# Kernel optimization log

Measured on AMD Instinct MI355X. Metric: run time of the kernel, lower is better.

Reference implementation:

```python
import jax, jax.numpy as jnp
import numpy as np

B, N, D, OUT = 32, 4096, 512, 512
LN_EPS = 1e-5
EPS = 1e-8


def _layernorm(x, g, b):
    m = jnp.mean(x, axis=-1, keepdims=True)
    v = jnp.mean((x - m) ** 2, axis=-1, keepdims=True)
    return (x - m) * jax.lax.rsqrt(v + LN_EPS) * g + b


def setup_inputs() -> dict:
    key = jax.random.key(0)
    ks = jax.random.split(key, 12)
    x = jax.random.normal(ks[0], (B, N, D), dtype=jnp.float32)
    mask = jax.random.bernoulli(ks[1], 0.9, (B, N))
    mask = mask.at[:, 0].set(True)  # guarantee no fully-masked row
    h = D // 4
    s = lambda fan_in: 1.0 / np.sqrt(fan_in)
    return {
        "x": x,
        "mask": mask,
        # attention MLP: Linear(D, D//4) -> tanh -> Linear(D//4, 1)
        "attn_w1": jax.random.normal(ks[2], (D, h), jnp.float32) * s(D),
        "attn_b1": jnp.zeros((h,), jnp.float32),
        "attn_w2": jax.random.normal(ks[3], (h, 1), jnp.float32) * s(h),
        "attn_b2": jnp.zeros((1,), jnp.float32),
        # gate: Linear(3D, D) -> LN -> GELU -> Linear(D, 3) -> softmax
        "gate_w1": jax.random.normal(ks[4], (3 * D, D), jnp.float32) * s(3 * D),
        "gate_b1": jnp.zeros((D,), jnp.float32),
        "gate_ln_g": jnp.ones((D,), jnp.float32),
        "gate_ln_b": jnp.zeros((D,), jnp.float32),
        "gate_w2": jax.random.normal(ks[5], (D, 3), jnp.float32) * s(D),
        "gate_b2": jnp.zeros((3,), jnp.float32),
        # out_proj: Linear(D, OUT) -> LN -> Dropout(eval: identity)
        "out_w": jax.random.normal(ks[6], (D, OUT), jnp.float32) * s(D),
        "out_b": jnp.zeros((OUT,), jnp.float32),
        "out_ln_g": jnp.ones((OUT,), jnp.float32),
        "out_ln_b": jnp.zeros((OUT,), jnp.float32),
    }


def reference(x, mask, attn_w1, attn_b1, attn_w2, attn_b2,
              gate_w1, gate_b1, gate_ln_g, gate_ln_b, gate_w2, gate_b2,
              out_w, out_b, out_ln_g, out_ln_b):
    # attention scores: [B, N]
    h = jnp.tanh(jnp.einsum('bnd,dh->bnh', x, attn_w1) + attn_b1)
    scores = (jnp.einsum('bnh,ho->bno', h, attn_w2) + attn_b2)[..., 0]
    scores = jnp.where(mask, scores, -jnp.inf)
    attn_w = jax.nn.softmax(scores, axis=-1)
    attn_w = jnp.nan_to_num(attn_w, nan=0.0)
    attn_pooled = jnp.einsum('bnd,bn->bd', x, attn_w)

    # masked max pool
    x_masked = jnp.where(mask[..., None], x, -jnp.inf)
    max_pooled = jnp.max(x_masked, axis=1)
    max_pooled = jnp.nan_to_num(max_pooled, nan=0.0, posinf=0.0, neginf=0.0)

    # masked mean pool
    mfl = mask.astype(x.dtype)
    masked_sum = jnp.einsum('bnd,bn->bd', x, mfl)
    num_valid = jnp.clip(jnp.sum(mfl, axis=1, keepdims=True), EPS, None)
    mean_pooled = masked_sum / num_valid

    # gated combine
    combined = jnp.concatenate([attn_pooled, max_pooled, mean_pooled], axis=-1)
    g = combined @ gate_w1 + gate_b1
    g = _layernorm(g, gate_ln_g, gate_ln_b)
    g = jax.nn.gelu(g, approximate=False)
    gates = jax.nn.softmax(g @ gate_w2 + gate_b2, axis=-1)  # [B, 3]

    stacked = jnp.stack([attn_pooled, max_pooled, mean_pooled], axis=2)  # [B, D, 3]
    weighted = jnp.einsum('bdk,bk->bd', stacked, gates)

    out = weighted @ out_w + out_b
    out = _layernorm(out, out_ln_g, out_ln_b)  # dropout: eval mode -> identity
    return out
```

## Files before the change

### kernel.cpp

```cpp
#include <hip/hip_runtime.h>
#include <hip/hip_bf16.h>
#include <math.h>

#define BB 32
#define NN 4096
#define DD 512
#define HH 128
#define NCH 128
#define LN_EPS 1e-5f
#define MEPS 1e-8f

typedef __attribute__((ext_vector_type(8))) short bf16x8;
typedef __attribute__((ext_vector_type(4))) float f32x4;

__device__ __forceinline__ unsigned pk_bf16(float a, float b) {
    unsigned ua = __float_as_uint(a); ua = (ua + 0x7FFFu + ((ua >> 16) & 1u)) >> 16;
    unsigned ub = __float_as_uint(b); ub = (ub + 0x7FFFu + ((ub >> 16) & 1u)) >> 16;
    return ua | (ub << 16);
}
__device__ __forceinline__ unsigned short bf16_1(float a) {
    unsigned ua = __float_as_uint(a);
    return (unsigned short)((ua + 0x7FFFu + ((ua >> 16) & 1u)) >> 16);
}
__device__ __forceinline__ float bflo(unsigned u) { return __uint_as_float(u << 16); }
__device__ __forceinline__ float bfhi(unsigned u) { return __uint_as_float(u & 0xFFFF0000u); }

__global__ __launch_bounds__(256) void gmsp_prep(
    const void* __restrict__ mask, unsigned char* __restrict__ m8,
    const float* __restrict__ w1, unsigned short* __restrict__ w1f)
{
    int blk = blockIdx.x, t = threadIdx.x;
    if (blk < 512) {
        __shared__ int sf[2];
        const unsigned* mu = (const unsigned*)mask;
        bool f32f = false, i8f = false;
#pragma unroll
        for (int i = 0; i < 4; ++i) {
            unsigned v = mu[t + i * 256];
            f32f |= (v == 0x3F800000u);
            i8f  |= (v > 1u) && (v != 0x3F800000u);
        }
        if (t == 0) { sf[0] = 0; sf[1] = 0; }
        __syncthreads();
        int wf32 = __any((int)f32f), wi8 = __any((int)i8f);
        if ((t & 63) == 0) {
            if (wf32) atomicOr(&sf[0], 1);
            if (wi8)  atomicOr(&sf[1], 1);
        }
        __syncthreads();
        int fmt = sf[0] ? 2 : (sf[1] ? 1 : 0);
        int i = blk * 256 + t;
        unsigned char v;
        if (fmt == 1)      v = ((const unsigned char*)mask)[i] != 0;
        else if (fmt == 2) v = ((const float*)mask)[i] != 0.0f;
        else               v = ((const int*)mask)[i] != 0;
        m8[i] = v;
    } else {
        int idx = (blk - 512) * 256 + t;
        int j = idx & 7;
        int e = idx >> 3;
        int lane = e & 63;
        int half = (e >> 6) & 1;
        int s = (e >> 7) & 15;
        int g2 = (e >> 11) & 3;
        int h = g2 * 32 + half * 16 + (lane & 15);
        int k = s * 32 + (lane >> 4) * 8 + j;
        w1f[(size_t)e * 8 + j] = bf16_1(w1[(size_t)k * HH + h]);
    }
}

__global__ __launch_bounds__(256, 1) void gmsp_fused(
    const float* __restrict__ x, const unsigned short* __restrict__ w1f,
    const float* __restrict__ b1, const float* __restrict__ w2,
    const float* __restrict__ b2, const unsigned char* __restrict__ m8,
    float* __restrict__ attnp, float* __restrict__ sump, float* __restrict__ maxp,
    float* __restrict__ mc, float* __restrict__ sc, float* __restrict__ cnt)
{
    __shared__ char At[32 * 1024];
    __shared__ float sred[32][4] __attribute__((aligned(16)));
    __shared__ float wrow[32];
    __shared__ float cpool[2][512];

    const int t = threadIdx.x;
    const int lane = t & 63, wid = t >> 6;
    const int l15 = lane & 15, lq = (lane >> 4) & 3;
    const int blk = blockIdx.x;
    const int b = blk >> 7, ch = blk & 127;
    const size_t row0 = (size_t)b * NN + (size_t)ch * 32;

    float4 sreg[16];
    {
        const float4* xb = (const float4*)(x + row0 * DD);
#pragma unroll
        for (int j = 0; j < 16; ++j) sreg[j] = xb[j * 256 + t];
    }
    uint4 mq0 = *(const uint4*)(m8 + row0);
    uint4 mq1 = *(const uint4*)(m8 + row0 + 16);
    unsigned mwa[8] = {mq0.x, mq0.y, mq0.z, mq0.w, mq1.x, mq1.y, mq1.z, mq1.w};

    const int H = t >> 7;
    const int c4 = t & 127;
    float ps[4] = {0.f, 0.f, 0.f, 0.f};
    float pm[4] = {-INFINITY, -INFINITY, -INFINITY, -INFINITY};
#pragma unroll
    for (int j = 0; j < 16; ++j) {
        const int row = 2 * j + H;
        float4 v = sreg[j];
        uint2 pw; pw.x = pk_bf16(v.x, v.y); pw.y = pk_bf16(v.z, v.w);
        *(uint2*)(At + row * 1024 + ((c4 * 8) ^ ((row & 7) << 4))) = pw;
        int mv = (mwa[j >> 1] >> ((2 * (j & 1) + H) * 8)) & 0xFF;
        if (mv) {
            ps[0] += v.x; ps[1] += v.y; ps[2] += v.z; ps[3] += v.w;
            pm[0] = fmaxf(pm[0], v.x); pm[1] = fmaxf(pm[1], v.y);
            pm[2] = fmaxf(pm[2], v.z); pm[3] = fmaxf(pm[3], v.w);
        }
    }
    __syncthreads();

    const int hb = wid * 32;
    f32x4 acc00 = (f32x4)0.f, acc01 = (f32x4)0.f, acc10 = (f32x4)0.f, acc11 = (f32x4)0.f;
    {
        const char* wf = (const char*)w1f + (size_t)wid * 32768 + (size_t)lane * 16;
        const char* ar0 = At + l15 * 1024;
        const char* ar1 = At + (16 + l15) * 1024;
        const int swz = (l15 & 7) << 4;
#pragma unroll
        for (int s = 0; s < 16; ++s) {
            bf16x8 bf0 = *(const bf16x8*)(wf + s * 2048);
            bf16x8 bf1 = *(const bf16x8*)(wf + s * 2048 + 1024);
            const int co = (s * 64 + lq * 16) ^ swz;
            bf16x8 a0 = *(const bf16x8*)(ar0 + co);
            bf16x8 a1 = *(const bf16x8*)(ar1 + co);
            acc00 = __builtin_amdgcn_mfma_f32_16x16x32_bf16(a0, bf0, acc00, 0, 0, 0);
            acc01 = __builtin_amdgcn_mfma_f32_16x16x32_bf16(a0, bf1, acc01, 0, 0, 0);
            acc10 = __builtin_amdgcn_mfma_f32_16x16x32_bf16(a1, bf0, acc10, 0, 0, 0);
            acc11 = __builtin_amdgcn_mfma_f32_16x16x32_bf16(a1, bf1, acc11, 0, 0, 0);
        }
    }
    {
        const float b10 = b1[hb + l15], b11 = b1[hb + 16 + l15];
        const float w20 = w2[hb + l15], w21 = w2[hb + 16 + l15];
#pragma unroll
        for (int rf = 0; rf < 2; ++rf) {
            f32x4 aA = rf ? acc10 : acc00;
            f32x4 aB = rf ? acc11 : acc01;
#pragma unroll
            for (int r = 0; r < 4; ++r) {
                float p0 = fminf(fmaxf(aA[r] + b10, -10.f), 10.f);
                float p1 = fminf(fmaxf(aB[r] + b11, -10.f), 10.f);
                float e0 = __expf(2.f * p0), e1 = __expf(2.f * p1);
                float v = (e0 - 1.f) / (e0 + 1.f) * w20 + (e1 - 1.f) / (e1 + 1.f) * w21;
                v += __shfl_xor(v, 1); v += __shfl_xor(v, 2);
                v += __shfl_xor(v, 4); v += __shfl_xor(v, 8);
                if (l15 == 0) sred[rf * 16 + lq * 4 + r][wid] = v;
            }
        }
    }
    __syncthreads();

    if (t < 32) {
        float4 s4 = *(const float4*)&sred[t][0];
        float ssum = s4.x + s4.y + s4.z + s4.w + b2[0];
        int valid = m8[row0 + t];
        float score = valid ? ssum : -INFINITY;
        float mx = score;
        mx = fmaxf(mx, __shfl_xor(mx, 1));  mx = fmaxf(mx, __shfl_xor(mx, 2));
        mx = fmaxf(mx, __shfl_xor(mx, 4));  mx = fmaxf(mx, __shfl_xor(mx, 8));
        mx = fmaxf(mx, __shfl_xor(mx, 16));
        float e = valid ? __expf(score - mx) : 0.f;
        wrow[t] = e;
        float ts = e, tc = valid ? 1.f : 0.f;
        ts += __shfl_xor(ts, 1);  tc += __shfl_xor(tc, 1);
        ts += __shfl_xor(ts, 2);  tc += __shfl_xor(tc, 2);
        ts += __shfl_xor(ts, 4);  tc += __shfl_xor(tc, 4);
        ts += __shfl_xor(ts, 8);  tc += __shfl_xor(tc, 8);
        ts += __shfl_xor(ts, 16); tc += __shfl_xor(tc, 16);
        if (t == 0) { mc[blk] = mx; sc[blk] = ts; cnt[blk] = tc; }
    }
    __syncthreads();

    float a0 = 0.f, a1 = 0.f;
#pragma unroll 8
    for (int r = 0; r < 32; ++r) {
        float w = wrow[r];
        unsigned u = *(const unsigned*)(At + r * 1024 + ((t * 4) ^ ((r & 7) << 4)));
        a0 = fmaf(w, bflo(u), a0);
        a1 = fmaf(w, bfhi(u), a1);
    }

    *(float4*)&cpool[H][c4 * 4] = make_float4(ps[0], ps[1], ps[2], ps[3]);
    __syncthreads();
    float sv0 = cpool[0][2 * t] + cpool[1][2 * t];
    float sv1 = cpool[0][2 * t + 1] + cpool[1][2 * t + 1];
    __syncthreads();
    *(float4*)&cpool[H][c4 * 4] = make_float4(pm[0], pm[1], pm[2], pm[3]);
    __syncthreads();
    float mv0 = fmaxf(cpool[0][2 * t], cpool[1][2 * t]);
    float mv1 = fmaxf(cpool[0][2 * t + 1], cpool[1][2 * t + 1]);

    const size_t ob = (size_t)blk * DD + 2 * t;
    *(float2*)(attnp + ob) = make_float2(a0, a1);
    *(float2*)(sump + ob)  = make_float2(sv0, sv1);
    *(float2*)(maxp + ob)  = make_float2(mv0, mv1);
}

__device__ __forceinline__ float gmsp_block_sum(float v, float* red, int t) {
    __syncthreads();
    red[t] = v; __syncthreads();
    for (int s = 128; s > 0; s >>= 1) { if (t < s) red[t] += red[t + s]; __syncthreads(); }
    return red[0];
}
__device__ __forceinline__ float gmsp_block_max(float v, float* red, int t) {
    __syncthreads();
    red[t] = v; __syncthreads();
    for (int s = 128; s > 0; s >>= 1) { if (t < s) red[t] = fmaxf(red[t], red[t + s]); __syncthreads(); }
    return red[0];
}

__global__ __launch_bounds__(256) void gmsp_tail(
    const float* __restrict__ attnp, const float* __restrict__ sump,
    const float* __restrict__ maxp, const float* __restrict__ mc,
    const float* __restrict__ sc, const float* __restrict__ cnt,
    const float* __restrict__ gate_w1, const float* __restrict__ gate_b1,
    const float* __restrict__ gln_g, const float* __restrict__ gln_b,
    const float* __restrict__ gate_w2, const float* __restrict__ gate_b2,
    const float* __restrict__ out_w, const float* __restrict__ out_b,
    const float* __restrict__ oln_g, const float* __restrict__ oln_b,
    float* __restrict__ out)
{
    __shared__ float comb[3 * DD];
    __shared__ float wvec[DD];
    __shared__ float red[256];
    __shared__ float ef[NCH];
    __shared__ float part[2][DD];
    int b = blockIdx.x, t = threadIdx.x;

    float mcv = (t < NCH) ? mc[b * NCH + t] : -INFINITY;
    float M = gmsp_block_max(mcv, red, t);
    float e = (t < NCH && mcv != -INFINITY) ? __expf(mcv - M) : 0.f;
    if (t < NCH) ef[t] = e;
    float T = gmsp_block_sum(e * ((t < NCH) ? sc[b * NCH + t] : 0.f), red, t);
    float C = gmsp_block_sum((t < NCH) ? cnt[b * NCH + t] : 0.f, red, t);
    float invT = T > 0.f ? 1.f / T : 0.f;
    C = fmaxf(C, MEPS);
    __syncthreads();

    int d0 = 2 * t;
    float ax = 0.f, ay = 0.f, sx = 0.f, sy = 0.f, mx = -INFINITY, my = -INFINITY;
    for (int c = 0; c < NCH; ++c) {
        size_t base = (size_t)(b * NCH + c) * DD + d0;
        float2 av = *(const float2*)(attnp + base);
        float2 sv = *(const float2*)(sump + base);
        float2 xv = *(const float2*)(maxp + base);
        float ec = ef[c];
        ax = fmaf(ec, av.x, ax); ay = fmaf(ec, av.y, ay);
        sx += sv.x; sy += sv.y;
        mx = fmaxf(mx, xv.x); my = fmaxf(my, xv.y);
    }
    ax *= invT; ay *= invT;
    float icnt = 1.f / C;
    float meanx = sx * icnt, meany = sy * icnt;
    if (isinf(mx)) mx = 0.f;
    if (isinf(my)) my = 0.f;

    comb[d0] = ax;               comb[d0 + 1] = ay;
    comb[DD + d0] = mx;          comb[DD + d0 + 1] = my;
    comb[2 * DD + d0] = meanx;   comb[2 * DD + d0 + 1] = meany;
    __syncthreads();

    const int th = t & 127, kh = t >> 7;
    {
        float4 g4 = make_float4(0.f, 0.f, 0.f, 0.f);
        const float* gw = gate_w1 + (size_t)kh * 768 * DD + th * 4;
        for (int k = 0; k < 768; ++k) {
            float cv = comb[kh * 768 + k];
            float4 wv = *(const float4*)(gw + (size_t)k * DD);
            g4.x = fmaf(cv, wv.x, g4.x); g4.y = fmaf(cv, wv.y, g4.y);
            g4.z = fmaf(cv, wv.z, g4.z); g4.w = fmaf(cv, wv.w, g4.w);
        }
        *(float4*)&part[kh][th * 4] = g4;
    }
    __syncthreads();
    float gx = part[0][d0] + part[1][d0] + gate_b1[d0];
    float gy = part[0][d0 + 1] + part[1][d0 + 1] + gate_b1[d0 + 1];

    float mg = gmsp_block_sum(gx + gy, red, t) * (1.f / DD);
    float vg = gmsp_block_sum(gx * gx + gy * gy, red, t) * (1.f / DD) - mg * mg;
    float inv = rsqrtf(vg + LN_EPS);
    gx = (gx - mg) * inv * gln_g[d0] + gln_b[d0];
    gy = (gy - mg) * inv * gln_g[d0 + 1] + gln_b[d0 + 1];
    gx = 0.5f * gx * (1.f + erff(gx * 0.70710678118654752f));
    gy = 0.5f * gy * (1.f + erff(gy * 0.70710678118654752f));

    float p0 = gx * gate_w2[d0 * 3 + 0] + gy * gate_w2[(d0 + 1) * 3 + 0];
    float p1 = gx * gate_w2[d0 * 3 + 1] + gy * gate_w2[(d0 + 1) * 3 + 1];
    float p2 = gx * gate_w2[d0 * 3 + 2] + gy * gate_w2[(d0 + 1) * 3 + 2];
    float l0 = gmsp_block_sum(p0, red, t) + gate_b2[0];
    float l1 = gmsp_block_sum(p1, red, t) + gate_b2[1];
    float l2 = gmsp_block_sum(p2, red, t) + gate_b2[2];
    float mxl = fmaxf(l0, fmaxf(l1, l2));
    float e0 = __expf(l0 - mxl), e1 = __expf(l1 - mxl), e2 = __expf(l2 - mxl);
    float ie = 1.f / (e0 + e1 + e2);
    float gw0 = e0 * ie, gw1 = e1 * ie, gw2 = e2 * ie;

    wvec[d0]     = ax * gw0 + mx * gw1 + meanx * gw2;
    wvec[d0 + 1] = ay * gw0 + my * gw1 + meany * gw2;
    __syncthreads();

    {
        float4 o4 = make_float4(0.f, 0.f, 0.f, 0.f);
        const float* ow = out_w + (size_t)kh * 256 * DD + th * 4;
        for (int k = 0; k < 256; ++k) {
            float wvk = wvec[kh * 256 + k];
            float4 w4 = *(const float4*)(ow + (size_t)k * DD);
            o4.x = fmaf(wvk, w4.x, o4.x); o4.y = fmaf(wvk, w4.y, o4.y);
            o4.z = fmaf(wvk, w4.z, o4.z); o4.w = fmaf(wvk, w4.w, o4.w);
        }
        *(float4*)&part[kh][th * 4] = o4;
    }
    __syncthreads();
    float ox = part[0][d0] + part[1][d0] + out_b[d0];
    float oy = part[0][d0 + 1] + part[1][d0 + 1] + out_b[d0 + 1];

    float mo = gmsp_block_sum(ox + oy, red, t) * (1.f / DD);
    float vo = gmsp_block_sum(ox * ox + oy * oy, red, t) * (1.f / DD) - mo * mo;
    float io = rsqrtf(vo + LN_EPS);
    float2 res;
    res.x = (ox - mo) * io * oln_g[d0] + oln_b[d0];
    res.y = (oy - mo) * io * oln_g[d0 + 1] + oln_b[d0 + 1];
    *(float2*)(out + (size_t)b * DD + d0) = res;
}

extern "C" void kernel_launch(void* const* d_in, const int* in_sizes, int n_in,
                              void* d_out, int out_size, void* d_ws, size_t ws_size,
                              hipStream_t stream) {
    const float* x        = (const float*)d_in[0];
    const void*  mask     = d_in[1];
    const float* attn_w1  = (const float*)d_in[2];
    const float* attn_b1  = (const float*)d_in[3];
    const float* attn_w2  = (const float*)d_in[4];
    const float* attn_b2  = (const float*)d_in[5];
    const float* gate_w1  = (const float*)d_in[6];
    const float* gate_b1  = (const float*)d_in[7];
    const float* gln_g    = (const float*)d_in[8];
    const float* gln_b    = (const float*)d_in[9];
    const float* gate_w2  = (const float*)d_in[10];
    const float* gate_b2  = (const float*)d_in[11];
    const float* out_w    = (const float*)d_in[12];
    const float* out_b    = (const float*)d_in[13];
    const float* oln_g    = (const float*)d_in[14];
    const float* oln_b    = (const float*)d_in[15];
    float* out = (float*)d_out;

    char* p = (char*)d_ws;
    unsigned char* m8 = (unsigned char*)p;      p += (size_t)BB * NN;
    unsigned short* w1f = (unsigned short*)p;   p += (size_t)DD * HH * 2;
    float* attnp = (float*)p;                   p += (size_t)BB * NCH * DD * 4;
    float* sump = (float*)p;                    p += (size_t)BB * NCH * DD * 4;
    float* maxp = (float*)p;                    p += (size_t)BB * NCH * DD * 4;
    float* mc = (float*)p;                      p += (size_t)BB * NCH * 4;
    float* sc = (float*)p;                      p += (size_t)BB * NCH * 4;
    float* cnt = (float*)p;                     p += (size_t)BB * NCH * 4;

    gmsp_prep<<<768, 256, 0, stream>>>(mask, m8, attn_w1, w1f);
    gmsp_fused<<<BB * NCH, 256, 0, stream>>>(x, w1f, attn_b1, attn_w2, attn_b2, m8,
                                             attnp, sump, maxp, mc, sc, cnt);
    gmsp_tail<<<BB, 256, 0, stream>>>(attnp, sump, maxp, mc, sc, cnt,
                                      gate_w1, gate_b1, gln_g, gln_b, gate_w2, gate_b2,
                                      out_w, out_b, oln_g, oln_b, out);
}
```

Before: 154.3 us.

## Halve rows per block to 16 and reuse LDS for pooling to raise occupancy

Each fused block now handles 16 rows instead of 32, doubling the grid to 8192 blocks. Launch bounds are raised to allow 8 blocks per CU. Shared memory is cut by sizing the staging tile for 16 rows and reusing it as the pooling reduction buffer, and the MFMA work per wave drops to one row tile. The goal is more resident waves to hide the latency of streaming x. The cost is twice as many partial rows for the tail kernel to reduce, plus less MFMA reuse of each loaded weight fragment.

Result: slower. 181.0 us (+17.3%).

```diff
diff --git a/kernel.cpp b/kernel.cpp
--- a/kernel.cpp
+++ b/kernel.cpp
@@ -6,7 +6,7 @@
 #define NN 4096
 #define DD 512
 #define HH 128
-#define NCH 128
+#define NCH 256
 #define LN_EPS 1e-5f
 #define MEPS 1e-8f
 
@@ -69,41 +69,39 @@
     }
 }
 
-__global__ __launch_bounds__(256, 1) void gmsp_fused(
+__global__ __launch_bounds__(256, 8) void gmsp_fused(
     const float* __restrict__ x, const unsigned short* __restrict__ w1f,
     const float* __restrict__ b1, const float* __restrict__ w2,
     const float* __restrict__ b2, const unsigned char* __restrict__ m8,
     float* __restrict__ attnp, float* __restrict__ sump, float* __restrict__ maxp,
     float* __restrict__ mc, float* __restrict__ sc, float* __restrict__ cnt)
 {
-    __shared__ char At[32 * 1024];
-    __shared__ float sred[32][4] __attribute__((aligned(16)));
-    __shared__ float wrow[32];
-    __shared__ float cpool[2][512];
+    __shared__ char At[16 * 1024];
+    __shared__ float sred[16][4] __attribute__((aligned(16)));
+    __shared__ float wrow[16];
 
     const int t = threadIdx.x;
     const int lane = t & 63, wid = t >> 6;
     const int l15 = lane & 15, lq = (lane >> 4) & 3;
     const int blk = blockIdx.x;
-    const int b = blk >> 7, ch = blk & 127;
-    const size_t row0 = (size_t)b * NN + (size_t)ch * 32;
-
-    float4 sreg[16];
+    const int b = blk >> 8, ch = blk & 255;
+    const size_t row0 = (size_t)b * NN + (size_t)ch * 16;
+
+    float4 sreg[8];
     {
         const float4* xb = (const float4*)(x + row0 * DD);
 #pragma unroll
-        for (int j = 0; j < 16; ++j) sreg[j] = xb[j * 256 + t];
-    }
-    uint4 mq0 = *(const uint4*)(m8 + row0);
-    uint4 mq1 = *(const uint4*)(m8 + row0 + 16);
-    unsigned mwa[8] = {mq0.x, mq0.y, mq0.z, mq0.w, mq1.x, mq1.y, mq1.z, mq1.w};
+        for (int j = 0; j < 8; ++j) sreg[j] = xb[j * 256 + t];
+    }
+    uint4 mq = *(const uint4*)(m8 + row0);
+    unsigned mwa[4] = {mq.x, mq.y, mq.z, mq.w};
 
     const int H = t >> 7;
     const int c4 = t & 127;
     float ps[4] = {0.f, 0.f, 0.f, 0.f};
     float pm[4] = {-INFINITY, -INFINITY, -INFINITY, -INFINITY};
 #pragma unroll
-    for (int j = 0; j < 16; ++j) {
+    for (int j = 0; j < 8; ++j) {
         const int row = 2 * j + H;
         float4 v = sreg[j];
         uint2 pw; pw.x = pk_bf16(v.x, v.y); pw.y = pk_bf16(v.z, v.w);
@@ -118,47 +116,37 @@
     __syncthreads();
 
     const int hb = wid * 32;
-    f32x4 acc00 = (f32x4)0.f, acc01 = (f32x4)0.f, acc10 = (f32x4)0.f, acc11 = (f32x4)0.f;
+    f32x4 acc0 = (f32x4)0.f, acc1 = (f32x4)0.f;
     {
         const char* wf = (const char*)w1f + (size_t)wid * 32768 + (size_t)lane * 16;
-        const char* ar0 = At + l15 * 1024;
-        const char* ar1 = At + (16 + l15) * 1024;
+        const char* ar = At + l15 * 1024;
         const int swz = (l15 & 7) << 4;
 #pragma unroll
         for (int s = 0; s < 16; ++s) {
             bf16x8 bf0 = *(const bf16x8*)(wf + s * 2048);
             bf16x8 bf1 = *(const bf16x8*)(wf + s * 2048 + 1024);
-            const int co = (s * 64 + lq * 16) ^ swz;
-            bf16x8 a0 = *(const bf16x8*)(ar0 + co);
-            bf16x8 a1 = *(const bf16x8*)(ar1 + co);
-            acc00 = __builtin_amdgcn_mfma_f32_16x16x32_bf16(a0, bf0, acc00, 0, 0, 0);
-            acc01 = __builtin_amdgcn_mfma_f32_16x16x32_bf16(a0, bf1, acc01, 0, 0, 0);
-            acc10 = __builtin_amdgcn_mfma_f32_16x16x32_bf16(a1, bf0, acc10, 0, 0, 0);
-            acc11 = __builtin_amdgcn_mfma_f32_16x16x32_bf16(a1, bf1, acc11, 0, 0, 0);
+            bf16x8 a0 = *(const bf16x8*)(ar + ((s * 64 + lq * 16) ^ swz));
+            acc0 = __builtin_amdgcn_mfma_f32_16x16x32_bf16(a0, bf0, acc0, 0, 0, 0);
+            acc1 = __builtin_amdgcn_mfma_f32_16x16x32_bf16(a0, bf1, acc1, 0, 0, 0);
         }
     }
     {
         const float b10 = b1[hb + l15], b11 = b1[hb + 16 + l15];
         const float w20 = w2[hb + l15], w21 = w2[hb + 16 + l15];
 #pragma unroll
-        for (int rf = 0; rf < 2; ++rf) {
-            f32x4 aA = rf ? acc10 : acc00;
-            f32x4 aB = rf ? acc11 : acc01;
-#pragma unroll
-            for (int r = 0; r < 4; ++r) {
-                float p0 = fminf(fmaxf(aA[r] + b10, -10.f), 10.f);
-                float p1 = fminf(fmaxf(aB[r] + b11, -10.f), 10.f);
-                float e0 = __expf(2.f * p0), e1 = __expf(2.f * p1);
-                float v = (e0 - 1.f) / (e0 + 1.f) * w20 + (e1 - 1.f) / (e1 + 1.f) * w21;
-                v += __shfl_xor(v, 1); v += __shfl_xor(v, 2);
-                v += __shfl_xor(v, 4); v += __shfl_xor(v, 8);
-                if (l15 == 0) sred[rf * 16 + lq * 4 + r][wid] = v;
-            }
-        }
-    }
-    __syncthreads();
-
-    if (t < 32) {
+        for (int r = 0; r < 4; ++r) {
+            float p0 = fminf(fmaxf(acc0[r] + b10, -10.f), 10.f);
+            float p1 = fminf(fmaxf(acc1[r] + b11, -10.f), 10.f);
+            float e0 = __expf(2.f * p0), e1 = __expf(2.f * p1);
+            float v = (e0 - 1.f) / (e0 + 1.f) * w20 + (e1 - 1.f) / (e1 + 1.f) * w21;
+            v += __shfl_xor(v, 1); v += __shfl_xor(v, 2);
+            v += __shfl_xor(v, 4); v += __shfl_xor(v, 8);
+            if (l15 == 0) sred[lq * 4 + r][wid] = v;
+        }
+    }
+    __syncthreads();
+
+    if (t < 16) {
         float4 s4 = *(const float4*)&sred[t][0];
         float ssum = s4.x + s4.y + s4.z + s4.w + b2[0];
         int valid = m8[row0 + t];
@@ -166,7 +154,6 @@
         float mx = score;
         mx = fmaxf(mx, __shfl_xor(mx, 1));  mx = fmaxf(mx, __shfl_xor(mx, 2));
         mx = fmaxf(mx, __shfl_xor(mx, 4));  mx = fmaxf(mx, __shfl_xor(mx, 8));
-        mx = fmaxf(mx, __shfl_xor(mx, 16));
         float e = valid ? __expf(score - mx) : 0.f;
         wrow[t] = e;
         float ts = e, tc = valid ? 1.f : 0.f;
@@ -174,29 +161,30 @@
         ts += __shfl_xor(ts, 2);  tc += __shfl_xor(tc, 2);
         ts += __shfl_xor(ts, 4);  tc += __shfl_xor(tc, 4);
         ts += __shfl_xor(ts, 8);  tc += __shfl_xor(tc, 8);
-        ts += __shfl_xor(ts, 16); tc += __shfl_xor(tc, 16);
         if (t == 0) { mc[blk] = mx; sc[blk] = ts; cnt[blk] = tc; }
     }
     __syncthreads();
 
     float a0 = 0.f, a1 = 0.f;
-#pragma unroll 8
-    for (int r = 0; r < 32; ++r) {
+#pragma unroll
+    for (int r = 0; r < 16; ++r) {
         float w = wrow[r];
         unsigned u = *(const unsigned*)(At + r * 1024 + ((t * 4) ^ ((r & 7) << 4)));
         a0 = fmaf(w, bflo(u), a0);
         a1 = fmaf(w, bfhi(u), a1);
     }
-
-    *(float4*)&cpool[H][c4 * 4] = make_float4(ps[0], ps[1], ps[2], ps[3]);
-    __syncthreads();
-    float sv0 = cpool[0][2 * t] + cpool[1][2 * t];
-    float sv1 = cpool[0][2 * t + 1] + cpool[1][2 * t + 1];
-    __syncthreads();
-    *(float4*)&cpool[H][c4 * 4] = make_float4(pm[0], pm[1], pm[2], pm[3]);
-    __syncthreads();
-    float mv0 = fmaxf(cpool[0][2 * t], cpool[1][2 * t]);
-    float mv1 = fmaxf(cpool[0][2 * t + 1], cpool[1][2 * t + 1]);
+    __syncthreads();
+
+    float* cpool = (float*)At;
+    *(float4*)&cpool[H * 512 + c4 * 4] = make_float4(ps[0], ps[1], ps[2], ps[3]);
+    __syncthreads();
+    float sv0 = cpool[2 * t] + cpool[512 + 2 * t];
+    float sv1 = cpool[2 * t + 1] + cpool[512 + 2 * t + 1];
+    __syncthreads();
+    *(float4*)&cpool[H * 512 + c4 * 4] = make_float4(pm[0], pm[1], pm[2], pm[3]);
+    __syncthreads();
+    float mv0 = fmaxf(cpool[2 * t], cpool[512 + 2 * t]);
+    float mv1 = fmaxf(cpool[2 * t + 1], cpool[512 + 2 * t + 1]);
 
     const size_t ob = (size_t)blk * DD + 2 * t;
     *(float2*)(attnp + ob) = make_float2(a0, a1);
@@ -235,12 +223,12 @@
     __shared__ float part[2][DD];
     int b = blockIdx.x, t = threadIdx.x;
 
-    float mcv = (t < NCH) ? mc[b * NCH + t] : -INFINITY;
+    float mcv = mc[b * NCH + t];
     float M = gmsp_block_max(mcv, red, t);
-    float e = (t < NCH && mcv != -INFINITY) ? __expf(mcv - M) : 0.f;
-    if (t < NCH) ef[t] = e;
-    float T = gmsp_block_sum(e * ((t < NCH) ? sc[b * NCH + t] : 0.f), red, t);
-    float C = gmsp_block_sum((t < NCH) ? cnt[b * NCH + t] : 0.f, red, t);
+    float e = (mcv != -INFINITY) ? __expf(mcv - M) : 0.f;
+    ef[t] = e;
+    float T = gmsp_block_sum(e * sc[b * NCH + t], red, t);
+    float C = gmsp_block_sum(cnt[b * NCH + t], red, t);
     float invT = T > 0.f ? 1.f / T : 0.f;
     C = fmaxf(C, MEPS);
     __syncthreads();
```
